# Kernel optimization log

Hardware: AMD Instinct MI355X
Metric: run time of the kernel (lower is better)

The kernel has to match this reference:

```python
import jax, jax.numpy as jnp
import numpy as np

B, L, K, D = 32, 1024, 1024, 1024

def setup_inputs() -> dict:
    key = jax.random.key(0)
    k1, k2, k3, k4, k5 = jax.random.split(key, 5)
    query = jax.random.normal(k1, (B, L, D), dtype=jnp.float32)
    context = jax.random.normal(k2, (B, K, D), dtype=jnp.float32)
    mask = jax.random.randint(k3, (B * L, K), 0, 2, dtype=jnp.int32)
    W_in = jax.random.normal(k4, (D, D), dtype=jnp.float32) * (D ** -0.5)
    W_out = jax.random.normal(k5, (D, 2 * D), dtype=jnp.float32) * ((2 * D) ** -0.5)
    return {"query": query, "context": context, "mask": mask, "W_in": W_in, "W_out": W_out}

def reference(query, context, mask, W_in, W_out):
    b, l, d = query.shape
    k = context.shape[1]
    # linear_in (general attention): q @ W_in.T
    q = jnp.einsum('bld,ed->ble', query, W_in)
    # attention scores [b, l, k]
    scores = jnp.einsum('bld,bkd->blk', q, context)
    # multiplicative-mask softmax with renormalization (masked_softmax, non-memory-efficient path)
    m = mask.astype(scores.dtype).reshape(b, l, k)
    w = jax.nn.softmax(scores * m, axis=-1) * m
    w = w / (jnp.sum(w, axis=-1, keepdims=True) + 1e-13)
    # mix attended context, concat with transformed query, project, tanh
    mix = jnp.einsum('blk,bkd->bld', w, context)
    combined = jnp.concatenate([mix, q], axis=-1)          # [b, l, 2d]
    out = jnp.tanh(jnp.einsum('blc,dc->bld', combined, W_out))
    return out
```

## Files before the change

### kernel.cpp

```cpp
#include <hip/hip_runtime.h>
#include <math.h>

typedef __bf16 bf16_t;
typedef __bf16 bf16x4 __attribute__((ext_vector_type(4)));
typedef __bf16 bf16x8 __attribute__((ext_vector_type(8)));
typedef _Float16 f16x4 __attribute__((ext_vector_type(4)));
typedef _Float16 f16x8 __attribute__((ext_vector_type(8)));
typedef float f32x4 __attribute__((ext_vector_type(4)));
typedef int i32x4 __attribute__((ext_vector_type(4)));

#define MFMA_BF16 __builtin_amdgcn_mfma_f32_16x16x32_bf16
#define MFMA_F16  __builtin_amdgcn_mfma_f32_16x16x32_f16

#define P_PRE                                         \
    __builtin_amdgcn_sched_barrier(0);                \
    __builtin_amdgcn_s_barrier();                     \
    asm volatile("s_waitcnt lgkmcnt(0)" ::: "memory");\
    __builtin_amdgcn_sched_barrier(0);                \
    __builtin_amdgcn_s_setprio(1)
#define P_POST                                        \
    __builtin_amdgcn_s_setprio(0);                    \
    __builtin_amdgcn_sched_barrier(0);                \
    __builtin_amdgcn_s_barrier()


__device__ __forceinline__ bf16_t to_bf16_rne(float x, float& rep) {
    unsigned u = __builtin_bit_cast(unsigned, x);
    unsigned r = u + 0x7fffu + ((u >> 16) & 1u);
    unsigned short h = (unsigned short)(r >> 16);
    rep = __builtin_bit_cast(float, ((unsigned)h) << 16);
    return __builtin_bit_cast(bf16_t, h);
}

__device__ __forceinline__ void g2l16(const void* g, void* l) {
    __builtin_amdgcn_global_load_lds(
        (const __attribute__((address_space(1))) unsigned int*)g,
        (__attribute__((address_space(3))) unsigned int*)l, 16, 0, 0);
}

__device__ __forceinline__ int lch(int r, int j) {
    return (r * 8 + (j ^ (r & 7))) * 8;
}

template <typename T>
__device__ __forceinline__ void stageA4(const T* __restrict__ gA, long long ldA,
                                        T* buf, int tid) {
    int wid = tid >> 6, lane = tid & 63;
#pragma unroll
    for (int i = 0; i < 4; ++i) {
        int cb = i * 512 + wid * 64;
        int c = cb + lane;
        int r = c >> 3, j = (c & 7) ^ (r & 7);
        g2l16(gA + (long long)r * ldA + j * 8, buf + (size_t)cb * 8);
    }
}

template <typename T>
__device__ __forceinline__ void stageB4(const T* __restrict__ gB, long long ldB,
                                        T* buf, int tid) {
    int wid = tid >> 6, lane = tid & 63;
#pragma unroll
    for (int i = 0; i < 4; ++i) {
        int cb = i * 512 + wid * 64;
        int c = cb + lane;
        int r = c >> 3, j = (c & 7) ^ (r & 7);
        g2l16(gB + (long long)r * ldB + j * 8, buf + 16384 + (size_t)cb * 8);
    }
}

template <typename T>
__device__ __forceinline__ void stage2(const T* __restrict__ gA, long long ldA,
                                       const T* __restrict__ gB, long long ldB,
                                       T* buf, int tid) {
    stageA4(gA, ldA, buf, tid);
    stageB4(gB, ldB, buf, tid);
}


__global__ __launch_bounds__(256) void split_int_k(const float* __restrict__ in,
                                                   bf16_t* __restrict__ out,
                                                   long long n4) {
    long long i = (long long)blockIdx.x * 256 + threadIdx.x;
    if (i >= n4) return;
    f32x4 v = ((const f32x4*)in)[i];
    bf16x4 hv, lv;
#pragma unroll
    for (int j = 0; j < 4; ++j) {
        float rep;
        hv[j] = to_bf16_rne(v[j], rep);
        float res = v[j] - rep;
        float rep2;
        lv[j] = to_bf16_rne(res, rep2);
    }
    long long row = i >> 8;
    int k = (int)(i & 255) * 4;
    long long base = row * 2048 + ((k >> 5) << 6) + (k & 31);
    *(bf16x4*)(out + base) = hv;
    *(bf16x4*)(out + base + 32) = lv;
}

__global__ __launch_bounds__(256) void cast_f16_k(const float* __restrict__ in,
                                                  _Float16* __restrict__ o, long long n4) {
    long long i = (long long)blockIdx.x * 256 + threadIdx.x;
    if (i >= n4) return;
    f32x4 v = ((const f32x4*)in)[i];
    f16x4 h;
#pragma unroll
    for (int j = 0; j < 4; ++j) h[j] = (_Float16)v[j];
    ((f16x4*)o)[i] = h;
}

__global__ __launch_bounds__(256) void prep_ctx_k(const float* __restrict__ ctx,
                                                  bf16_t* __restrict__ ctx_int,
                                                  _Float16* __restrict__ ctxT) {
    __shared__ _Float16 tl[32][33];
    int b = blockIdx.z;
    int k0 = blockIdx.x * 32, d0 = blockIdx.y * 32;
    const float* src = ctx + ((long long)b * 1024 + k0) * 1024 + d0;
    int x = threadIdx.x, y = threadIdx.y;
#pragma unroll
    for (int i = 0; i < 4; ++i) {
        int k = y + i * 8;
        float v = src[(long long)k * 1024 + x];
        float rep;
        bf16_t hb = to_bf16_rne(v, rep);
        float rep2;
        bf16_t lb = to_bf16_rne(v - rep, rep2);
        long long rb = ((long long)b * 1024 + k0 + k) * 2048 + d0 * 2 + x;
        ctx_int[rb] = hb;
        ctx_int[rb + 32] = lb;
        tl[x][k] = (_Float16)v;
    }
    __syncthreads();
    _Float16* dst = ctxT + ((long long)b * 1024 + d0) * 1024 + k0;
#pragma unroll
    for (int i = 0; i < 4; ++i) {
        int dd = y + i * 8;
        dst[(long long)dd * 1024 + x] = tl[dd][x];
    }
}

__global__ __launch_bounds__(256) void masked_softmax_k(const float* __restrict__ s,
                                                        const int* __restrict__ m,
                                                        _Float16* __restrict__ w) {
    long long row = blockIdx.x;
    const f32x4* sr = (const f32x4*)(s + row * 1024);
    const i32x4* mr = (const i32x4*)(m + row * 1024);
    f16x4* wr_ = (f16x4*)(w + row * 1024);
    int t = threadIdx.x;
    int lane = t & 63, wid = t >> 6;
    f32x4 v = sr[t];
    i32x4 mk = mr[t];
    float mx = -3.0e38f;
#pragma unroll
    for (int i = 0; i < 4; ++i)
        if (mk[i]) mx = fmaxf(mx, v[i]);
#pragma unroll
    for (int off = 32; off; off >>= 1) mx = fmaxf(mx, __shfl_xor(mx, off));
    __shared__ float rm[4], rs[4];
    if (!lane) rm[wid] = mx;
    __syncthreads();
    mx = fmaxf(fmaxf(rm[0], rm[1]), fmaxf(rm[2], rm[3]));
    float sum = 0.f;
    f32x4 e;
#pragma unroll
    for (int i = 0; i < 4; ++i) {
        e[i] = mk[i] ? expf(v[i] - mx) : 0.f;
        sum += e[i];
    }
#pragma unroll
    for (int off = 32; off; off >>= 1) sum += __shfl_xor(sum, off);
    if (!lane) rs[wid] = sum;
    __syncthreads();
    sum = rs[0] + rs[1] + rs[2] + rs[3];
    float inv = sum > 0.f ? 1.0f / sum : 0.f;
    f16x4 o;
#pragma unroll
    for (int i = 0; i < 4; ++i) o[i] = (_Float16)(e[i] * inv);
    wr_[t] = o;
}

template <int EPI>
__global__ __launch_bounds__(512, 2) void gemm_x3_256(
    const bf16_t* __restrict__ Aint, const bf16_t* __restrict__ Bint,
    long long sA, long long sB, long long sC, int nbx, int nby,
    float* __restrict__ Cs, bf16_t* __restrict__ Qint, _Float16* __restrict__ Qf) {
    __shared__ bf16_t lds[65536];
    const int NT = 32;
    int tid = threadIdx.x, lane = tid & 63, wid = tid >> 6;
    int wr = wid >> 2, wc = wid & 3;
    int nwg = gridDim.x;
    int bid = blockIdx.x;
    int lid = (bid & 7) * (nwg >> 3) + (bid >> 3);
    int by = lid % nby;
    int t2_ = lid / nby;
    int bx = t2_ % nbx;
    int z = t2_ / nbx;
    const bf16_t* At = Aint + (long long)z * sA + (long long)bx * 256 * 2048;
    const bf16_t* Bt = Bint + (long long)z * sB + (long long)by * 256 * 2048;
    stage2(At, 2048ll, Bt, 2048ll, lds, tid);
    stage2(At + 64, 2048ll, Bt + 64, 2048ll, lds + 32768, tid);
    f32x4 acc[8][4] = {};
    int l15 = lane & 15, l4 = lane >> 4;
    asm volatile("s_waitcnt vmcnt(8)" ::: "memory");
    __builtin_amdgcn_sched_barrier(0);
    __builtin_amdgcn_s_barrier();
    for (int t = 0; t < NT; ++t) {
        bf16_t* buf = lds + (size_t)(t & 1) * 32768;
        bf16_t* bufB = buf + 16384;
        const bf16_t* At2 = At + (long long)(t + 2) * 64;
        const bf16_t* Bt2 = Bt + (long long)(t + 2) * 64;
        bool st = (t + 2 < NT);
        bf16x8 bh[4], bl[4], ahA[2], alA[2];
#pragma unroll
        for (int n = 0; n < 4; ++n) {
            int rB = wc * 64 + n * 16 + l15;
            bh[n] = *(const bf16x8*)(bufB + lch(rB, l4));
            bl[n] = *(const bf16x8*)(bufB + lch(rB, 4 + l4));
        }
#pragma unroll
        for (int i = 0; i < 2; ++i) {
            int rA = wr * 128 + i * 16 + l15;
            ahA[i] = *(const bf16x8*)(buf + lch(rA, l4));
            alA[i] = *(const bf16x8*)(buf + lch(rA, 4 + l4));
        }
        P_PRE;
#pragma unroll
        for (int i = 0; i < 2; ++i)
#pragma unroll
            for (int n = 0; n < 4; ++n) {
                f32x4 a = acc[i][n];
                a = MFMA_BF16(ahA[i], bh[n], a, 0, 0, 0);
                a = MFMA_BF16(ahA[i], bl[n], a, 0, 0, 0);
                a = MFMA_BF16(alA[i], bh[n], a, 0, 0, 0);
                acc[i][n] = a;
            }
        P_POST;
        bf16x8 ahB[2], alB[2], ahC[2], alC[2];
#pragma unroll
        for (int i = 0; i < 2; ++i) {
            int rA = wr * 128 + (2 + i) * 16 + l15;
            ahB[i] = *(const bf16x8*)(buf + lch(rA, l4));
            alB[i] = *(const bf16x8*)(buf + lch(rA, 4 + l4));
        }
#pragma unroll
        for (int i = 0; i < 2; ++i) {
            int rA = wr * 128 + (4 + i) * 16 + l15;
            ahC[i] = *(const bf16x8*)(buf + lch(rA, l4));
            alC[i] = *(const bf16x8*)(buf + lch(rA, 4 + l4));
        }
        P_PRE;
#pragma unroll
        for (int i = 0; i < 2; ++i)
#pragma unroll
            for (int n = 0; n < 4; ++n) {
                f32x4 a = acc[2 + i][n];
                a = MFMA_BF16(ahB[i], bh[n], a, 0, 0, 0);
                a = MFMA_BF16(ahB[i], bl[n], a, 0, 0, 0);
                a = MFMA_BF16(alB[i], bh[n], a, 0, 0, 0);
                acc[2 + i][n] = a;
            }
        P_POST;
        bf16x8 ahD[2], alD[2];
#pragma unroll
        for (int i = 0; i < 2; ++i) {
            int rA = wr * 128 + (6 + i) * 16 + l15;
            ahD[i] = *(const bf16x8*)(buf + lch(rA, l4));
            alD[i] = *(const bf16x8*)(buf + lch(rA, 4 + l4));
        }
        if (st) stageB4(Bt2, 2048ll, buf, tid);
        P_PRE;
#pragma unroll
        for (int i = 0; i < 2; ++i)
#pragma unroll
            for (int n = 0; n < 4; ++n) {
                f32x4 a = acc[4 + i][n];
                a = MFMA_BF16(ahC[i], bh[n], a, 0, 0, 0);
                a = MFMA_BF16(ahC[i], bl[n], a, 0, 0, 0);
                a = MFMA_BF16(alC[i], bh[n], a, 0, 0, 0);
                acc[4 + i][n] = a;
            }
        P_POST;
        if (st) stageA4(At2, 2048ll, buf, tid);
        __builtin_amdgcn_s_setprio(1);
#pragma unroll
        for (int i = 0; i < 2; ++i)
#pragma unroll
            for (int n = 0; n < 4; ++n) {
                f32x4 a = acc[6 + i][n];
                a = MFMA_BF16(ahD[i], bh[n], a, 0, 0, 0);
                a = MFMA_BF16(ahD[i], bl[n], a, 0, 0, 0);
                a = MFMA_BF16(alD[i], bh[n], a, 0, 0, 0);
                acc[6 + i][n] = a;
            }
        __builtin_amdgcn_s_setprio(0);
        __builtin_amdgcn_sched_barrier(0);
        if (t + 2 < NT) {
            asm volatile("s_waitcnt vmcnt(8)" ::: "memory");
        } else if (t + 1 < NT) {
            asm volatile("s_waitcnt vmcnt(0)" ::: "memory");
        }
        __builtin_amdgcn_sched_barrier(0);
        __builtin_amdgcn_s_barrier();
    }
    int r0 = bx * 256 + wr * 128 + (l4 << 2);
    int c0 = by * 256 + wc * 64 + l15;
#pragma unroll
    for (int m = 0; m < 8; ++m)
#pragma unroll
        for (int n = 0; n < 4; ++n)
#pragma unroll
            for (int j = 0; j < 4; ++j) {
                int r = r0 + m * 16 + j;
                int c = c0 + n * 16;
                float v = acc[m][n][j];
                if (EPI == 0) {
                    Cs[(long long)z * sC + (long long)r * 1024 + c] = v;
                } else {
                    float rep;
                    bf16_t hb = to_bf16_rne(v, rep);
                    float res = v - rep;
                    float rep2;
                    bf16_t lb = to_bf16_rne(res, rep2);
                    long long rb = (long long)r * 2048 + ((c >> 5) << 6) + (c & 31);
                    Qint[rb] = hb;
                    Qint[rb + 32] = lb;
                    Qf[(long long)r * 1024 + c] = (_Float16)v;
                }
            }
}

template <int EPI>
__global__ __launch_bounds__(512, 2) void gemm_f16_256(
    const _Float16* __restrict__ A1, const _Float16* __restrict__ A2,
    const _Float16* __restrict__ B,
    long long ldA, long long ldB, long long sA, long long sB, long long sC,
    int NT, int swt, int nbx, int nby,
    _Float16* __restrict__ Cm, float* __restrict__ Co) {
    __shared__ _Float16 lds[65536];
    int tid = threadIdx.x, lane = tid & 63, wid = tid >> 6;
    int wr = wid >> 2, wc = wid & 3;
    int nwg = gridDim.x;
    int bid = blockIdx.x;
    int lid = (bid & 7) * (nwg >> 3) + (bid >> 3);
    int by = lid % nby;
    int t2_ = lid / nby;
    int bx = t2_ % nbx;
    int z = t2_ / nbx;
    const _Float16* A1t = A1 + (long long)z * sA + (long long)bx * 256 * ldA;
    const _Float16* A2t = A2 + (long long)bx * 256 * ldA;
    const _Float16* Bt = B + (long long)z * sB + (long long)by * 256 * ldB;
    stage2((0 < swt) ? A1t : A2t, ldA, Bt, ldB, lds, tid);
    stage2((1 < swt) ? A1t + 64 : A2t + (long long)(1 - swt) * 64, ldA, Bt + 64, ldB,
           lds + 32768, tid);
    f32x4 acc[8][4] = {};
    int l15 = lane & 15, l4 = lane >> 4;
    asm volatile("s_waitcnt vmcnt(8)" ::: "memory");
    __builtin_amdgcn_sched_barrier(0);
    __builtin_amdgcn_s_barrier();
    for (int t = 0; t < NT; ++t) {
        _Float16* buf = lds + (size_t)(t & 1) * 32768;
        _Float16* bufB = buf + 16384;
        int tt = t + 2;
        bool st = (tt < NT);
        const _Float16* gA2 =
            (tt < swt) ? A1t + (long long)tt * 64 : A2t + (long long)(tt - swt) * 64;
        const _Float16* gB2 = Bt + (long long)tt * 64;
        f16x8 bfr[4][2], aA[2][2];
#pragma unroll
        for (int n = 0; n < 4; ++n) {
            int rB = wc * 64 + n * 16 + l15;
#pragma unroll
            for (int ks = 0; ks < 2; ++ks)
                bfr[n][ks] = *(const f16x8*)(bufB + lch(rB, ks * 4 + l4));
        }
#pragma unroll
        for (int i = 0; i < 2; ++i) {
            int rA = wr * 128 + i * 16 + l15;
#pragma unroll
            for (int ks = 0; ks < 2; ++ks)
                aA[i][ks] = *(const f16x8*)(buf + lch(rA, ks * 4 + l4));
        }
        P_PRE;
#pragma unroll
        for (int i = 0; i < 2; ++i)
#pragma unroll
            for (int n = 0; n < 4; ++n) {
                f32x4 v = acc[i][n];
                v = MFMA_F16(aA[i][0], bfr[n][0], v, 0, 0, 0);
                v = MFMA_F16(aA[i][1], bfr[n][1], v, 0, 0, 0);
                acc[i][n] = v;
            }
        P_POST;
        f16x8 aB[2][2], aC[2][2];
#pragma unroll
        for (int i = 0; i < 2; ++i) {
            int rA = wr * 128 + (2 + i) * 16 + l15;
#pragma unroll
            for (int ks = 0; ks < 2; ++ks)
                aB[i][ks] = *(const f16x8*)(buf + lch(rA, ks * 4 + l4));
        }
#pragma unroll
        for (int i = 0; i < 2; ++i) {
            int rA = wr * 128 + (4 + i) * 16 + l15;
#pragma unroll
            for (int ks = 0; ks < 2; ++ks)
                aC[i][ks] = *(const f16x8*)(buf + lch(rA, ks * 4 + l4));
        }
        P_PRE;
#pragma unroll
        for (int i = 0; i < 2; ++i)
#pragma unroll
            for (int n = 0; n < 4; ++n) {
                f32x4 v = acc[2 + i][n];
                v = MFMA_F16(aB[i][0], bfr[n][0], v, 0, 0, 0);
                v = MFMA_F16(aB[i][1], bfr[n][1], v, 0, 0, 0);
                acc[2 + i][n] = v;
            }
        P_POST;
        f16x8 aD[2][2];
#pragma unroll
        for (int i = 0; i < 2; ++i) {
            int rA = wr * 128 + (6 + i) * 16 + l15;
#pragma unroll
            for (int ks = 0; ks < 2; ++ks)
                aD[i][ks] = *(const f16x8*)(buf + lch(rA, ks * 4 + l4));
        }
        if (st) stageB4(gB2, ldB, buf, tid);
        P_PRE;
#pragma unroll
        for (int i = 0; i < 2; ++i)
#pragma unroll
            for (int n = 0; n < 4; ++n) {
                f32x4 v = acc[4 + i][n];
                v = MFMA_F16(aC[i][0], bfr[n][0], v, 0, 0, 0);
                v = MFMA_F16(aC[i][1], bfr[n][1], v, 0, 0, 0);
                acc[4 + i][n] = v;
            }
        P_POST;
        if (st) stageA4(gA2, ldA, buf, tid);
        __builtin_amdgcn_s_setprio(1);
#pragma unroll
        for (int i = 0; i < 2; ++i)
#pragma unroll
            for (int n = 0; n < 4; ++n) {
                f32x4 v = acc[6 + i][n];
                v = MFMA_F16(aD[i][0], bfr[n][0], v, 0, 0, 0);
                v = MFMA_F16(aD[i][1], bfr[n][1], v, 0, 0, 0);
                acc[6 + i][n] = v;
            }
        __builtin_amdgcn_s_setprio(0);
        __builtin_amdgcn_sched_barrier(0);
        if (t + 2 < NT) {
            asm volatile("s_waitcnt vmcnt(8)" ::: "memory");
        } else if (t + 1 < NT) {
            asm volatile("s_waitcnt vmcnt(0)" ::: "memory");
        }
        __builtin_amdgcn_sched_barrier(0);
        __builtin_amdgcn_s_barrier();
    }
    int r0 = bx * 256 + wr * 128 + (l4 << 2);
    int c0 = by * 256 + wc * 64 + l15;
#pragma unroll
    for (int m = 0; m < 8; ++m)
#pragma unroll
        for (int n = 0; n < 4; ++n)
#pragma unroll
            for (int j = 0; j < 4; ++j) {
                int r = r0 + m * 16 + j;
                int c = c0 + n * 16;
                float v = acc[m][n][j];
                if (EPI == 0) {
                    Cm[(long long)z * sC + (long long)r * 1024 + c] = (_Float16)v;
                } else {
                    Co[(long long)r * 1024 + c] = tanhf(v);
                }
            }
}


extern "C" void kernel_launch(void* const* d_in, const int* in_sizes, int n_in,
                              void* d_out, int out_size, void* d_ws, size_t ws_size,
                              hipStream_t stream) {
    const float* query = (const float*)d_in[0];
    const float* ctx = (const float*)d_in[1];
    const int* mask = (const int*)d_in[2];
    const float* Win = (const float*)d_in[3];
    const float* Wout = (const float*)d_in[4];
    float* outp = (float*)d_out;

    const long long MB = 1048576ll;
    int G = 1;
    if ((long long)ws_size >= 512 * MB) G = 32;
    else if ((long long)ws_size >= 256 * MB) G = 16;
    else if ((long long)ws_size >= 128 * MB) G = 8;
    else if ((long long)ws_size >= 64 * MB) G = 4;
    else if ((long long)ws_size >= 32 * MB) G = 2;

    char* p = (char*)d_ws;
    const long long R = (long long)G * 1024;
    bf16_t* qint = (bf16_t*)p; p += 4 * G * MB;
    _Float16* qf = (_Float16*)p; p += 2 * G * MB;
    char* slabA = p; p += 4 * G * MB;
    bf16_t* win_int = (bf16_t*)slabA;
    bf16_t* ctx_int = (bf16_t*)slabA;
    _Float16* wf = (_Float16*)slabA;
    _Float16* mixf = (_Float16*)(slabA + 2 * G * MB);
    _Float16* ctxT = (_Float16*)p; p += 2 * G * MB;
    char* slabC = p;
    bf16_t* qs_int = (bf16_t*)slabC;
    float* scores = (float*)slabC;
    _Float16* woutf = (_Float16*)slabC;

    const long long LD = 1048576ll;

    for (int b0 = 0; b0 < 32; b0 += G) {
        const float* qsrc = query + (long long)b0 * LD;
        const float* csrc = ctx + (long long)b0 * LD;
        split_int_k<<<1024, 256, 0, stream>>>(Win, win_int, 262144ll);
        split_int_k<<<(int)R, 256, 0, stream>>>(qsrc, qs_int, R * 256);
        gemm_x3_256<1><<<16 * G, 512, 0, stream>>>(
            qs_int, win_int, 0, 0, 0, 4 * G, 4, nullptr, qint, qf);
        prep_ctx_k<<<dim3(32, 32, G), dim3(32, 8, 1), 0, stream>>>(csrc, ctx_int, ctxT);
        gemm_x3_256<0><<<16 * G, 512, 0, stream>>>(
            qint, ctx_int, 2097152ll, 2097152ll, 1048576ll, 4, 4,
            scores, nullptr, nullptr);
        masked_softmax_k<<<(int)R, 256, 0, stream>>>(
            scores, mask + (long long)b0 * 1024 * 1024, wf);
        cast_f16_k<<<2048, 256, 0, stream>>>(Wout, woutf, 524288ll);
        gemm_f16_256<0><<<16 * G, 512, 0, stream>>>(
            wf, wf, ctxT, 1024ll, 1024ll, 1048576ll, 1048576ll, 1048576ll,
            16, 1 << 20, 4, 4, mixf, nullptr);
        gemm_f16_256<1><<<16 * G, 512, 0, stream>>>(
            mixf, qf, woutf, 1024ll, 2048ll, 0, 0, 0,
            32, 16, 4 * G, 4, nullptr, outp + (long long)b0 * LD);
    }
}
```

Before: 762.3 us.

## Replace per-phase barriers with lgkmcnt-pipelined LDS fragment loads in GEMM loops

Both GEMM main loops drop the workgroup barrier and full lgkmcnt(0) wait around each MFMA phase. A fragments for later phases are now issued ahead of time, and partial lgkmcnt waits let LDS reads overlap MFMAs of earlier phases. One barrier before the global-to-LDS staging of both A and B tiles replaces the two separate staging points. This cuts barrier stalls, but it moves all staging of the next tile into the final phase and raises register pressure from the extra in-flight fragments.

After: 783.8 us. 1.03x slower.

```diff
diff --git a/kernel.cpp b/kernel.cpp
--- a/kernel.cpp
+++ b/kernel.cpp
@@ -12,16 +12,12 @@
 #define MFMA_BF16 __builtin_amdgcn_mfma_f32_16x16x32_bf16
 #define MFMA_F16  __builtin_amdgcn_mfma_f32_16x16x32_f16
 
-#define P_PRE                                         \
-    __builtin_amdgcn_sched_barrier(0);                \
-    __builtin_amdgcn_s_barrier();                     \
-    asm volatile("s_waitcnt lgkmcnt(0)" ::: "memory");\
-    __builtin_amdgcn_sched_barrier(0);                \
-    __builtin_amdgcn_s_setprio(1)
-#define P_POST                                        \
-    __builtin_amdgcn_s_setprio(0);                    \
-    __builtin_amdgcn_sched_barrier(0);                \
-    __builtin_amdgcn_s_barrier()
+#define SB0 __builtin_amdgcn_sched_barrier(0)
+#define LGKM(n)                                                  \
+    do {                                                         \
+        asm volatile("s_waitcnt lgkmcnt(" #n ")" ::: "memory");  \
+        __builtin_amdgcn_sched_barrier(0);                       \
+    } while (0)
 
 
 __device__ __forceinline__ bf16_t to_bf16_rne(float x, float& rep) {
@@ -43,8 +39,9 @@
 }
 
 template <typename T>
-__device__ __forceinline__ void stageA4(const T* __restrict__ gA, long long ldA,
-                                        T* buf, int tid) {
+__device__ __forceinline__ void stage2(const T* __restrict__ gA, long long ldA,
+                                       const T* __restrict__ gB, long long ldB,
+                                       T* buf, int tid) {
     int wid = tid >> 6, lane = tid & 63;
 #pragma unroll
     for (int i = 0; i < 4; ++i) {
@@ -53,12 +50,6 @@
         int r = c >> 3, j = (c & 7) ^ (r & 7);
         g2l16(gA + (long long)r * ldA + j * 8, buf + (size_t)cb * 8);
     }
-}
-
-template <typename T>
-__device__ __forceinline__ void stageB4(const T* __restrict__ gB, long long ldB,
-                                        T* buf, int tid) {
-    int wid = tid >> 6, lane = tid & 63;
 #pragma unroll
     for (int i = 0; i < 4; ++i) {
         int cb = i * 512 + wid * 64;
@@ -66,14 +57,6 @@
         int r = c >> 3, j = (c & 7) ^ (r & 7);
         g2l16(gB + (long long)r * ldB + j * 8, buf + 16384 + (size_t)cb * 8);
     }
-}
-
-template <typename T>
-__device__ __forceinline__ void stage2(const T* __restrict__ gA, long long ldA,
-                                       const T* __restrict__ gB, long long ldB,
-                                       T* buf, int tid) {
-    stageA4(gA, ldA, buf, tid);
-    stageB4(gB, ldB, buf, tid);
 }
 
 
@@ -203,104 +186,115 @@
     f32x4 acc[8][4] = {};
     int l15 = lane & 15, l4 = lane >> 4;
     asm volatile("s_waitcnt vmcnt(8)" ::: "memory");
-    __builtin_amdgcn_sched_barrier(0);
+    SB0;
     __builtin_amdgcn_s_barrier();
     for (int t = 0; t < NT; ++t) {
         bf16_t* buf = lds + (size_t)(t & 1) * 32768;
         bf16_t* bufB = buf + 16384;
-        const bf16_t* At2 = At + (long long)(t + 2) * 64;
-        const bf16_t* Bt2 = Bt + (long long)(t + 2) * 64;
         bool st = (t + 2 < NT);
-        bf16x8 bh[4], bl[4], ahA[2], alA[2];
+        bf16x8 bh[4], bl[4];
 #pragma unroll
         for (int n = 0; n < 4; ++n) {
             int rB = wc * 64 + n * 16 + l15;
             bh[n] = *(const bf16x8*)(bufB + lch(rB, l4));
             bl[n] = *(const bf16x8*)(bufB + lch(rB, 4 + l4));
         }
+        bf16x8 ah0[2], al0[2];
 #pragma unroll
         for (int i = 0; i < 2; ++i) {
             int rA = wr * 128 + i * 16 + l15;
-            ahA[i] = *(const bf16x8*)(buf + lch(rA, l4));
-            alA[i] = *(const bf16x8*)(buf + lch(rA, 4 + l4));
-        }
-        P_PRE;
-#pragma unroll
-        for (int i = 0; i < 2; ++i)
-#pragma unroll
-            for (int n = 0; n < 4; ++n) {
-                f32x4 a = acc[i][n];
-                a = MFMA_BF16(ahA[i], bh[n], a, 0, 0, 0);
-                a = MFMA_BF16(ahA[i], bl[n], a, 0, 0, 0);
-                a = MFMA_BF16(alA[i], bh[n], a, 0, 0, 0);
-                acc[i][n] = a;
-            }
-        P_POST;
-        bf16x8 ahB[2], alB[2], ahC[2], alC[2];
+            ah0[i] = *(const bf16x8*)(buf + lch(rA, l4));
+            al0[i] = *(const bf16x8*)(buf + lch(rA, 4 + l4));
+        }
+        SB0;
+        bf16x8 ah1[2], al1[2];
 #pragma unroll
         for (int i = 0; i < 2; ++i) {
             int rA = wr * 128 + (2 + i) * 16 + l15;
-            ahB[i] = *(const bf16x8*)(buf + lch(rA, l4));
-            alB[i] = *(const bf16x8*)(buf + lch(rA, 4 + l4));
-        }
+            ah1[i] = *(const bf16x8*)(buf + lch(rA, l4));
+            al1[i] = *(const bf16x8*)(buf + lch(rA, 4 + l4));
+        }
+        SB0;
+        LGKM(4);
+        bf16x8 ah2[2], al2[2];
 #pragma unroll
         for (int i = 0; i < 2; ++i) {
             int rA = wr * 128 + (4 + i) * 16 + l15;
-            ahC[i] = *(const bf16x8*)(buf + lch(rA, l4));
-            alC[i] = *(const bf16x8*)(buf + lch(rA, 4 + l4));
-        }
-        P_PRE;
-#pragma unroll
-        for (int i = 0; i < 2; ++i)
-#pragma unroll
-            for (int n = 0; n < 4; ++n) {
-                f32x4 a = acc[2 + i][n];
-                a = MFMA_BF16(ahB[i], bh[n], a, 0, 0, 0);
-                a = MFMA_BF16(ahB[i], bl[n], a, 0, 0, 0);
-                a = MFMA_BF16(alB[i], bh[n], a, 0, 0, 0);
-                acc[2 + i][n] = a;
-            }
-        P_POST;
-        bf16x8 ahD[2], alD[2];
+            ah2[i] = *(const bf16x8*)(buf + lch(rA, l4));
+            al2[i] = *(const bf16x8*)(buf + lch(rA, 4 + l4));
+        }
+        SB0;
+        __builtin_amdgcn_s_setprio(1);
+#pragma unroll
+        for (int i = 0; i < 2; ++i)
+#pragma unroll
+            for (int n = 0; n < 4; ++n) {
+                f32x4 a = acc[i][n];
+                a = MFMA_BF16(ah0[i], bh[n], a, 0, 0, 0);
+                a = MFMA_BF16(ah0[i], bl[n], a, 0, 0, 0);
+                a = MFMA_BF16(al0[i], bh[n], a, 0, 0, 0);
+                acc[i][n] = a;
+            }
+        __builtin_amdgcn_s_setprio(0);
+        LGKM(4);
+        bf16x8 ah3[2], al3[2];
 #pragma unroll
         for (int i = 0; i < 2; ++i) {
             int rA = wr * 128 + (6 + i) * 16 + l15;
-            ahD[i] = *(const bf16x8*)(buf + lch(rA, l4));
-            alD[i] = *(const bf16x8*)(buf + lch(rA, 4 + l4));
-        }
-        if (st) stageB4(Bt2, 2048ll, buf, tid);
-        P_PRE;
+            ah3[i] = *(const bf16x8*)(buf + lch(rA, l4));
+            al3[i] = *(const bf16x8*)(buf + lch(rA, 4 + l4));
+        }
+        SB0;
+        __builtin_amdgcn_s_setprio(1);
+#pragma unroll
+        for (int i = 0; i < 2; ++i)
+#pragma unroll
+            for (int n = 0; n < 4; ++n) {
+                f32x4 a = acc[2 + i][n];
+                a = MFMA_BF16(ah1[i], bh[n], a, 0, 0, 0);
+                a = MFMA_BF16(ah1[i], bl[n], a, 0, 0, 0);
+                a = MFMA_BF16(al1[i], bh[n], a, 0, 0, 0);
+                acc[2 + i][n] = a;
+            }
+        __builtin_amdgcn_s_setprio(0);
+        LGKM(4);
+        __builtin_amdgcn_s_setprio(1);
 #pragma unroll
         for (int i = 0; i < 2; ++i)
 #pragma unroll
             for (int n = 0; n < 4; ++n) {
                 f32x4 a = acc[4 + i][n];
-                a = MFMA_BF16(ahC[i], bh[n], a, 0, 0, 0);
-                a = MFMA_BF16(ahC[i], bl[n], a, 0, 0, 0);
-                a = MFMA_BF16(alC[i], bh[n], a, 0, 0, 0);
+                a = MFMA_BF16(ah2[i], bh[n], a, 0, 0, 0);
+                a = MFMA_BF16(ah2[i], bl[n], a, 0, 0, 0);
+                a = MFMA_BF16(al2[i], bh[n], a, 0, 0, 0);
                 acc[4 + i][n] = a;
             }
-        P_POST;
-        if (st) stageA4(At2, 2048ll, buf, tid);
+        __builtin_amdgcn_s_setprio(0);
+        LGKM(0);
+        __builtin_amdgcn_s_barrier();
+        SB0;
+        if (st)
+            stage2(At + (long long)(t + 2) * 64, 2048ll,
+                   Bt + (long long)(t + 2) * 64, 2048ll, buf, tid);
         __builtin_amdgcn_s_setprio(1);
 #pragma unroll
         for (int i = 0; i < 2; ++i)
 #pragma unroll
             for (int n = 0; n < 4; ++n) {
                 f32x4 a = acc[6 + i][n];
-                a = MFMA_BF16(ahD[i], bh[n], a, 0, 0, 0);
-                a = MFMA_BF16(ahD[i], bl[n], a, 0, 0, 0);
-                a = MFMA_BF16(alD[i], bh[n], a, 0, 0, 0);
+                a = MFMA_BF16(ah3[i], bh[n], a, 0, 0, 0);
+                a = MFMA_BF16(ah3[i], bl[n], a, 0, 0, 0);
+                a = MFMA_BF16(al3[i], bh[n], a, 0, 0, 0);
                 acc[6 + i][n] = a;
             }
         __builtin_amdgcn_s_setprio(0);
-        __builtin_amdgcn_sched_barrier(0);
+        SB0;
         if (t + 2 < NT) {
             asm volatile("s_waitcnt vmcnt(8)" ::: "memory");
         } else if (t + 1 < NT) {
             asm volatile("s_waitcnt vmcnt(0)" ::: "memory");
         }
-        __builtin_amdgcn_sched_barrier(0);
+        SB0;
         __builtin_amdgcn_s_barrier();
     }
     int r0 = bx * 256 + wr * 128 + (l4 << 2);
@@ -356,7 +350,7 @@
     f32x4 acc[8][4] = {};
     int l15 = lane & 15, l4 = lane >> 4;
     asm volatile("s_waitcnt vmcnt(8)" ::: "memory");
-    __builtin_amdgcn_sched_barrier(0);
+    SB0;
     __builtin_amdgcn_s_barrier();
     for (int t = 0; t < NT; ++t) {
         _Float16* buf = lds + (size_t)(t & 1) * 32768;
@@ -366,7 +360,7 @@
         const _Float16* gA2 =
             (tt < swt) ? A1t + (long long)tt * 64 : A2t + (long long)(tt - swt) * 64;
         const _Float16* gB2 = Bt + (long long)tt * 64;
-        f16x8 bfr[4][2], aA[2][2];
+        f16x8 bfr[4][2];
 #pragma unroll
         for (int n = 0; n < 4; ++n) {
             int rB = wc * 64 + n * 16 + l15;
@@ -374,89 +368,100 @@
             for (int ks = 0; ks < 2; ++ks)
                 bfr[n][ks] = *(const f16x8*)(bufB + lch(rB, ks * 4 + l4));
         }
-#pragma unroll
-        for (int i = 0; i < 2; ++i) {
-            int rA = wr * 128 + i * 16 + l15;
-#pragma unroll
-            for (int ks = 0; ks < 2; ++ks)
-                aA[i][ks] = *(const f16x8*)(buf + lch(rA, ks * 4 + l4));
-        }
-        P_PRE;
+        f16x8 a0[2][2];
+#pragma unroll
+        for (int i = 0; i < 2; ++i)
+#pragma unroll
+            for (int ks = 0; ks < 2; ++ks) {
+                int rA = wr * 128 + i * 16 + l15;
+                a0[i][ks] = *(const f16x8*)(buf + lch(rA, ks * 4 + l4));
+            }
+        SB0;
+        f16x8 a1[2][2];
+#pragma unroll
+        for (int i = 0; i < 2; ++i)
+#pragma unroll
+            for (int ks = 0; ks < 2; ++ks) {
+                int rA = wr * 128 + (2 + i) * 16 + l15;
+                a1[i][ks] = *(const f16x8*)(buf + lch(rA, ks * 4 + l4));
+            }
+        SB0;
+        LGKM(4);
+        f16x8 a2[2][2];
+#pragma unroll
+        for (int i = 0; i < 2; ++i)
+#pragma unroll
+            for (int ks = 0; ks < 2; ++ks) {
+                int rA = wr * 128 + (4 + i) * 16 + l15;
+                a2[i][ks] = *(const f16x8*)(buf + lch(rA, ks * 4 + l4));
+            }
+        SB0;
+        __builtin_amdgcn_s_setprio(1);
 #pragma unroll
         for (int i = 0; i < 2; ++i)
 #pragma unroll
             for (int n = 0; n < 4; ++n) {
                 f32x4 v = acc[i][n];
-                v = MFMA_F16(aA[i][0], bfr[n][0], v, 0, 0, 0);
-                v = MFMA_F16(aA[i][1], bfr[n][1], v, 0, 0, 0);
+                v = MFMA_F16(a0[i][0], bfr[n][0], v, 0, 0, 0);
+                v = MFMA_F16(a0[i][1], bfr[n][1], v, 0, 0, 0);
                 acc[i][n] = v;
             }
-        P_POST;
-        f16x8 aB[2][2], aC[2][2];
-#pragma unroll
-        for (int i = 0; i < 2; ++i) {
-            int rA = wr * 128 + (2 + i) * 16 + l15;
-#pragma unroll
-            for (int ks = 0; ks < 2; ++ks)
-                aB[i][ks] = *(const f16x8*)(buf + lch(rA, ks * 4 + l4));
-        }
-#pragma unroll
-        for (int i = 0; i < 2; ++i) {
-            int rA = wr * 128 + (4 + i) * 16 + l15;
-#pragma unroll
-            for (int ks = 0; ks < 2; ++ks)
-                aC[i][ks] = *(const f16x8*)(buf + lch(rA, ks * 4 + l4));
-        }
-        P_PRE;
+        __builtin_amdgcn_s_setprio(0);
+        LGKM(4);
+        f16x8 a3[2][2];
+#pragma unroll
+        for (int i = 0; i < 2; ++i)
+#pragma unroll
+            for (int ks = 0; ks < 2; ++ks) {
+                int rA = wr * 128 + (6 + i) * 16 + l15;
+                a3[i][ks] = *(const f16x8*)(buf + lch(rA, ks * 4 + l4));
+            }
+        SB0;
+        __builtin_amdgcn_s_setprio(1);
 #pragma unroll
         for (int i = 0; i < 2; ++i)
 #pragma unroll
             for (int n = 0; n < 4; ++n) {
                 f32x4 v = acc[2 + i][n];
-                v = MFMA_F16(aB[i][0], bfr[n][0], v, 0, 0, 0);
-                v = MFMA_F16(aB[i][1], bfr[n][1], v, 0, 0, 0);
+                v = MFMA_F16(a1[i][0], bfr[n][0], v, 0, 0, 0);
+                v = MFMA_F16(a1[i][1], bfr[n][1], v, 0, 0, 0);
                 acc[2 + i][n] = v;
             }
-        P_POST;
-        f16x8 aD[2][2];
-#pragma unroll
-        for (int i = 0; i < 2; ++i) {
-            int rA = wr * 128 + (6 + i) * 16 + l15;
-#pragma unroll
-            for (int ks = 0; ks < 2; ++ks)
-                aD[i][ks] = *(const f16x8*)(buf + lch(rA, ks * 4 + l4));
-        }
-        if (st) stageB4(gB2, ldB, buf, tid);
-        P_PRE;
+        __builtin_amdgcn_s_setprio(0);
+        LGKM(4);
+        __builtin_amdgcn_s_setprio(1);
 #pragma unroll
         for (int i = 0; i < 2; ++i)
 #pragma unroll
             for (int n = 0; n < 4; ++n) {
                 f32x4 v = acc[4 + i][n];
-                v = MFMA_F16(aC[i][0], bfr[n][0], v, 0, 0, 0);
-                v = MFMA_F16(aC[i][1], bfr[n][1], v, 0, 0, 0);
+                v = MFMA_F16(a2[i][0], bfr[n][0], v, 0, 0, 0);
+                v = MFMA_F16(a2[i][1], bfr[n][1], v, 0, 0, 0);
                 acc[4 + i][n] = v;
             }
-        P_POST;
-        if (st) stageA4(gA2, ldA, buf, tid);
+        __builtin_amdgcn_s_setprio(0);
+        LGKM(0);
+        __builtin_amdgcn_s_barrier();
+        SB0;
+        if (st) stage2(gA2, ldA, gB2, ldB, buf, tid);
         __builtin_amdgcn_s_setprio(1);
 #pragma unroll
         for (int i = 0; i < 2; ++i)
 #pragma unroll
             for (int n = 0; n < 4; ++n) {
                 f32x4 v = acc[6 + i][n];
-                v = MFMA_F16(aD[i][0], bfr[n][0], v, 0, 0, 0);
-                v = MFMA_F16(aD[i][1], bfr[n][1], v, 0, 0, 0);
+                v = MFMA_F16(a3[i][0], bfr[n][0], v, 0, 0, 0);
+                v = MFMA_F16(a3[i][1], bfr[n][1], v, 0, 0, 0);
                 acc[6 + i][n] = v;
             }
         __builtin_amdgcn_s_setprio(0);
-        __builtin_amdgcn_sched_barrier(0);
+        SB0;
         if (t + 2 < NT) {
             asm volatile("s_waitcnt vmcnt(8)" ::: "memory");
         } else if (t + 1 < NT) {
             asm volatile("s_waitcnt vmcnt(0)" ::: "memory");
         }
-        __builtin_amdgcn_sched_barrier(0);
+        SB0;
         __builtin_amdgcn_s_barrier();
     }
     int r0 = bx * 256 + wr * 128 + (l4 << 2);
```

## Fuse fp32-to-bf16 split into x3 GEMM loads and mask into scores epilogue

Applied to the files above, without the earlier changes.

The x3 bf16 GEMM now loads fp32 query/context tiles directly into registers and splits them into hi/lo bf16 while writing LDS. This removes the separate split_int_k pass over query and the ctx_int output of the context prep kernel. The mask is applied in the scores GEMM epilogue by writing a large negative sentinel, so the softmax kernel no longer reads the mask. The cost is more VALU work and register-staged loads inside the GEMM main loop, a changed vmcnt pipeline, and reordered workspace buffers.

New measurement: 781.3 us. +2.5%, slower.

```diff
diff --git a/kernel.cpp b/kernel.cpp
--- a/kernel.cpp
+++ b/kernel.cpp
@@ -11,6 +11,7 @@
 
 #define MFMA_BF16 __builtin_amdgcn_mfma_f32_16x16x32_bf16
 #define MFMA_F16  __builtin_amdgcn_mfma_f32_16x16x32_f16
+#define SB0 __builtin_amdgcn_sched_barrier(0)
 
 #define P_PRE                                         \
     __builtin_amdgcn_sched_barrier(0);                \
@@ -42,9 +43,47 @@
     return (r * 8 + (j ^ (r & 7))) * 8;
 }
 
-template <typename T>
-__device__ __forceinline__ void stageA4(const T* __restrict__ gA, long long ldA,
-                                        T* buf, int tid) {
+__device__ __forceinline__ void stageG(const bf16_t* __restrict__ g, bf16_t* dst,
+                                       int tid) {
+    int wid = tid >> 6, lane = tid & 63;
+#pragma unroll
+    for (int i = 0; i < 4; ++i) {
+        int cb = i * 512 + wid * 64;
+        int c = cb + lane;
+        int r = c >> 3, j = (c & 7) ^ (r & 7);
+        g2l16(g + (long long)r * 2048 + j * 8, dst + (size_t)cb * 8);
+    }
+}
+
+__device__ __forceinline__ void ldf32(const float* __restrict__ g, int tid,
+                                      f32x4* v) {
+    int r = tid >> 1, h = tid & 1;
+    const f32x4* s = (const f32x4*)(g + (long long)r * 1024 + h * 16);
+#pragma unroll
+    for (int i = 0; i < 4; ++i) v[i] = s[i];
+}
+
+__device__ __forceinline__ void wrsplit(bf16_t* dst, int tid, const f32x4* v) {
+    int r = tid >> 1, h = tid & 1;
+    bf16x8 H[2], L[2];
+#pragma unroll
+    for (int e = 0; e < 16; ++e) {
+        float x = v[e >> 2][e & 3];
+        float rep;
+        bf16_t hb = to_bf16_rne(x, rep);
+        float r2;
+        bf16_t lb = to_bf16_rne(x - rep, r2);
+        H[e >> 3][e & 7] = hb;
+        L[e >> 3][e & 7] = lb;
+    }
+    *(bf16x8*)(dst + lch(r, h * 2)) = H[0];
+    *(bf16x8*)(dst + lch(r, h * 2 + 1)) = H[1];
+    *(bf16x8*)(dst + lch(r, 4 + h * 2)) = L[0];
+    *(bf16x8*)(dst + lch(r, 4 + h * 2 + 1)) = L[1];
+}
+
+__device__ __forceinline__ void stageA4h(const _Float16* __restrict__ gA, long long ldA,
+                                         _Float16* buf, int tid) {
     int wid = tid >> 6, lane = tid & 63;
 #pragma unroll
     for (int i = 0; i < 4; ++i) {
@@ -54,10 +93,8 @@
         g2l16(gA + (long long)r * ldA + j * 8, buf + (size_t)cb * 8);
     }
 }
-
-template <typename T>
-__device__ __forceinline__ void stageB4(const T* __restrict__ gB, long long ldB,
-                                        T* buf, int tid) {
+__device__ __forceinline__ void stageB4h(const _Float16* __restrict__ gB, long long ldB,
+                                         _Float16* buf, int tid) {
     int wid = tid >> 6, lane = tid & 63;
 #pragma unroll
     for (int i = 0; i < 4; ++i) {
@@ -67,13 +104,11 @@
         g2l16(gB + (long long)r * ldB + j * 8, buf + 16384 + (size_t)cb * 8);
     }
 }
-
-template <typename T>
-__device__ __forceinline__ void stage2(const T* __restrict__ gA, long long ldA,
-                                       const T* __restrict__ gB, long long ldB,
-                                       T* buf, int tid) {
-    stageA4(gA, ldA, buf, tid);
-    stageB4(gB, ldB, buf, tid);
+__device__ __forceinline__ void stage2h(const _Float16* __restrict__ gA, long long ldA,
+                                        const _Float16* __restrict__ gB, long long ldB,
+                                        _Float16* buf, int tid) {
+    stageA4h(gA, ldA, buf, tid);
+    stageB4h(gB, ldB, buf, tid);
 }
 
 
@@ -110,9 +145,8 @@
     ((f16x4*)o)[i] = h;
 }
 
-__global__ __launch_bounds__(256) void prep_ctx_k(const float* __restrict__ ctx,
-                                                  bf16_t* __restrict__ ctx_int,
-                                                  _Float16* __restrict__ ctxT) {
+__global__ __launch_bounds__(256) void transpose_ctx_k(const float* __restrict__ ctx,
+                                                       _Float16* __restrict__ ctxT) {
     __shared__ _Float16 tl[32][33];
     int b = blockIdx.z;
     int k0 = blockIdx.x * 32, d0 = blockIdx.y * 32;
@@ -121,15 +155,7 @@
 #pragma unroll
     for (int i = 0; i < 4; ++i) {
         int k = y + i * 8;
-        float v = src[(long long)k * 1024 + x];
-        float rep;
-        bf16_t hb = to_bf16_rne(v, rep);
-        float rep2;
-        bf16_t lb = to_bf16_rne(v - rep, rep2);
-        long long rb = ((long long)b * 1024 + k0 + k) * 2048 + d0 * 2 + x;
-        ctx_int[rb] = hb;
-        ctx_int[rb + 32] = lb;
-        tl[x][k] = (_Float16)v;
+        tl[x][k] = (_Float16)src[(long long)k * 1024 + x];
     }
     __syncthreads();
     _Float16* dst = ctxT + ((long long)b * 1024 + d0) * 1024 + k0;
@@ -141,20 +167,14 @@
 }
 
 __global__ __launch_bounds__(256) void masked_softmax_k(const float* __restrict__ s,
-                                                        const int* __restrict__ m,
                                                         _Float16* __restrict__ w) {
     long long row = blockIdx.x;
     const f32x4* sr = (const f32x4*)(s + row * 1024);
-    const i32x4* mr = (const i32x4*)(m + row * 1024);
     f16x4* wr_ = (f16x4*)(w + row * 1024);
     int t = threadIdx.x;
     int lane = t & 63, wid = t >> 6;
     f32x4 v = sr[t];
-    i32x4 mk = mr[t];
-    float mx = -3.0e38f;
-#pragma unroll
-    for (int i = 0; i < 4; ++i)
-        if (mk[i]) mx = fmaxf(mx, v[i]);
+    float mx = fmaxf(fmaxf(v[0], v[1]), fmaxf(v[2], v[3]));
 #pragma unroll
     for (int off = 32; off; off >>= 1) mx = fmaxf(mx, __shfl_xor(mx, off));
     __shared__ float rm[4], rs[4];
@@ -165,7 +185,7 @@
     f32x4 e;
 #pragma unroll
     for (int i = 0; i < 4; ++i) {
-        e[i] = mk[i] ? expf(v[i] - mx) : 0.f;
+        e[i] = expf(v[i] - mx);
         sum += e[i];
     }
 #pragma unroll
@@ -173,17 +193,18 @@
     if (!lane) rs[wid] = sum;
     __syncthreads();
     sum = rs[0] + rs[1] + rs[2] + rs[3];
-    float inv = sum > 0.f ? 1.0f / sum : 0.f;
+    float inv = (mx < -1.0e38f) ? 0.f : 1.0f / sum;
     f16x4 o;
 #pragma unroll
     for (int i = 0; i < 4; ++i) o[i] = (_Float16)(e[i] * inv);
     wr_[t] = o;
 }
 
-template <int EPI>
+template <int EPI, bool F32A>
 __global__ __launch_bounds__(512, 2) void gemm_x3_256(
-    const bf16_t* __restrict__ Aint, const bf16_t* __restrict__ Bint,
-    long long sA, long long sB, long long sC, int nbx, int nby,
+    const bf16_t* __restrict__ Gint, const float* __restrict__ Fsrc,
+    const int* __restrict__ Mk,
+    long long sG, long long sF, long long sC, int nbx, int nby,
     float* __restrict__ Cs, bf16_t* __restrict__ Qint, _Float16* __restrict__ Qf) {
     __shared__ bf16_t lds[65536];
     const int NT = 32;
@@ -196,21 +217,31 @@
     int t2_ = lid / nby;
     int bx = t2_ % nbx;
     int z = t2_ / nbx;
-    const bf16_t* At = Aint + (long long)z * sA + (long long)bx * 256 * 2048;
-    const bf16_t* Bt = Bint + (long long)z * sB + (long long)by * 256 * 2048;
-    stage2(At, 2048ll, Bt, 2048ll, lds, tid);
-    stage2(At + 64, 2048ll, Bt + 64, 2048ll, lds + 32768, tid);
+    const bf16_t* Gt = Gint + (long long)z * sG + (long long)(F32A ? by : bx) * 256 * 2048;
+    const float* Ft = Fsrc + (long long)z * sF + (long long)(F32A ? bx : by) * 256 * 1024;
+    const int FOFF = F32A ? 0 : 16384;
+    const int GOFF = F32A ? 16384 : 0;
+    {
+        f32x4 v[4];
+        ldf32(Ft, tid, v);
+        wrsplit(lds + FOFF, tid, v);
+        ldf32(Ft + 32, tid, v);
+        wrsplit(lds + 32768 + FOFF, tid, v);
+        stageG(Gt, lds + GOFF, tid);
+        stageG(Gt + 64, lds + 32768 + GOFF, tid);
+        asm volatile("s_waitcnt lgkmcnt(0) vmcnt(0)" ::: "memory");
+        SB0;
+        __builtin_amdgcn_s_barrier();
+    }
     f32x4 acc[8][4] = {};
     int l15 = lane & 15, l4 = lane >> 4;
-    asm volatile("s_waitcnt vmcnt(8)" ::: "memory");
-    __builtin_amdgcn_sched_barrier(0);
-    __builtin_amdgcn_s_barrier();
     for (int t = 0; t < NT; ++t) {
         bf16_t* buf = lds + (size_t)(t & 1) * 32768;
         bf16_t* bufB = buf + 16384;
-        const bf16_t* At2 = At + (long long)(t + 2) * 64;
-        const bf16_t* Bt2 = Bt + (long long)(t + 2) * 64;
         bool st = (t + 2 < NT);
+        f32x4 v[4];
+        if (st) ldf32(Ft + (t + 2) * 32, tid, v);
+        SB0;
         bf16x8 bh[4], bl[4], ahA[2], alA[2];
 #pragma unroll
         for (int n = 0; n < 4; ++n) {
@@ -268,7 +299,7 @@
             ahD[i] = *(const bf16x8*)(buf + lch(rA, l4));
             alD[i] = *(const bf16x8*)(buf + lch(rA, 4 + l4));
         }
-        if (st) stageB4(Bt2, 2048ll, buf, tid);
+        if (st && F32A) stageG(Gt + (long long)(t + 2) * 64, buf + GOFF, tid);
         P_PRE;
 #pragma unroll
         for (int i = 0; i < 2; ++i)
@@ -281,7 +312,8 @@
                 acc[4 + i][n] = a;
             }
         P_POST;
-        if (st) stageA4(At2, 2048ll, buf, tid);
+        if (st && !F32A) stageG(Gt + (long long)(t + 2) * 64, buf + GOFF, tid);
+        if (st) wrsplit(buf + FOFF, tid, v);
         __builtin_amdgcn_s_setprio(1);
 #pragma unroll
         for (int i = 0; i < 2; ++i)
@@ -294,17 +326,20 @@
                 acc[6 + i][n] = a;
             }
         __builtin_amdgcn_s_setprio(0);
-        __builtin_amdgcn_sched_barrier(0);
-        if (t + 2 < NT) {
-            asm volatile("s_waitcnt vmcnt(8)" ::: "memory");
-        } else if (t + 1 < NT) {
+        SB0;
+        asm volatile("s_waitcnt lgkmcnt(0)" ::: "memory");
+        SB0;
+        if (st) {
+            asm volatile("s_waitcnt vmcnt(4)" ::: "memory");
+        } else {
             asm volatile("s_waitcnt vmcnt(0)" ::: "memory");
         }
-        __builtin_amdgcn_sched_barrier(0);
+        SB0;
         __builtin_amdgcn_s_barrier();
     }
     int r0 = bx * 256 + wr * 128 + (l4 << 2);
     int c0 = by * 256 + wc * 64 + l15;
+    const int* mrow = (EPI == 0) ? (Mk + (long long)z * 1048576ll) : nullptr;
 #pragma unroll
     for (int m = 0; m < 8; ++m)
 #pragma unroll
@@ -315,7 +350,8 @@
                 int c = c0 + n * 16;
                 float v = acc[m][n][j];
                 if (EPI == 0) {
-                    Cs[(long long)z * sC + (long long)r * 1024 + c] = v;
+                    int mv = mrow[(long long)r * 1024 + c];
+                    Cs[(long long)z * sC + (long long)r * 1024 + c] = mv ? v : -3.0e38f;
                 } else {
                     float rep;
                     bf16_t hb = to_bf16_rne(v, rep);
@@ -350,13 +386,13 @@
     const _Float16* A1t = A1 + (long long)z * sA + (long long)bx * 256 * ldA;
     const _Float16* A2t = A2 + (long long)bx * 256 * ldA;
     const _Float16* Bt = B + (long long)z * sB + (long long)by * 256 * ldB;
-    stage2((0 < swt) ? A1t : A2t, ldA, Bt, ldB, lds, tid);
-    stage2((1 < swt) ? A1t + 64 : A2t + (long long)(1 - swt) * 64, ldA, Bt + 64, ldB,
-           lds + 32768, tid);
+    stage2h((0 < swt) ? A1t : A2t, ldA, Bt, ldB, lds, tid);
+    stage2h((1 < swt) ? A1t + 64 : A2t + (long long)(1 - swt) * 64, ldA, Bt + 64, ldB,
+            lds + 32768, tid);
     f32x4 acc[8][4] = {};
     int l15 = lane & 15, l4 = lane >> 4;
     asm volatile("s_waitcnt vmcnt(8)" ::: "memory");
-    __builtin_amdgcn_sched_barrier(0);
+    SB0;
     __builtin_amdgcn_s_barrier();
     for (int t = 0; t < NT; ++t) {
         _Float16* buf = lds + (size_t)(t & 1) * 32768;
@@ -386,10 +422,10 @@
         for (int i = 0; i < 2; ++i)
 #pragma unroll
             for (int n = 0; n < 4; ++n) {
-                f32x4 v = acc[i][n];
-                v = MFMA_F16(aA[i][0], bfr[n][0], v, 0, 0, 0);
-                v = MFMA_F16(aA[i][1], bfr[n][1], v, 0, 0, 0);
-                acc[i][n] = v;
+                f32x4 vv = acc[i][n];
+                vv = MFMA_F16(aA[i][0], bfr[n][0], vv, 0, 0, 0);
+                vv = MFMA_F16(aA[i][1], bfr[n][1], vv, 0, 0, 0);
+                acc[i][n] = vv;
             }
         P_POST;
         f16x8 aB[2][2], aC[2][2];
@@ -412,10 +448,10 @@
         for (int i = 0; i < 2; ++i)
 #pragma unroll
             for (int n = 0; n < 4; ++n) {
-                f32x4 v = acc[2 + i][n];
-                v = MFMA_F16(aB[i][0], bfr[n][0], v, 0, 0, 0);
-                v = MFMA_F16(aB[i][1], bfr[n][1], v, 0, 0, 0);
-                acc[2 + i][n] = v;
+                f32x4 vv = acc[2 + i][n];
+                vv = MFMA_F16(aB[i][0], bfr[n][0], vv, 0, 0, 0);
+                vv = MFMA_F16(aB[i][1], bfr[n][1], vv, 0, 0, 0);
+                acc[2 + i][n] = vv;
             }
         P_POST;
         f16x8 aD[2][2];
@@ -426,37 +462,37 @@
             for (int ks = 0; ks < 2; ++ks)
                 aD[i][ks] = *(const f16x8*)(buf + lch(rA, ks * 4 + l4));
         }
-        if (st) stageB4(gB2, ldB, buf, tid);
+        if (st) stageB4h(gB2, ldB, buf, tid);
         P_PRE;
 #pragma unroll
         for (int i = 0; i < 2; ++i)
 #pragma unroll
             for (int n = 0; n < 4; ++n) {
-                f32x4 v = acc[4 + i][n];
-                v = MFMA_F16(aC[i][0], bfr[n][0], v, 0, 0, 0);
-                v = MFMA_F16(aC[i][1], bfr[n][1], v, 0, 0, 0);
-                acc[4 + i][n] = v;
+                f32x4 vv = acc[4 + i][n];
+                vv = MFMA_F16(aC[i][0], bfr[n][0], vv, 0, 0, 0);
+                vv = MFMA_F16(aC[i][1], bfr[n][1], vv, 0, 0, 0);
+                acc[4 + i][n] = vv;
             }
         P_POST;
-        if (st) stageA4(gA2, ldA, buf, tid);
+        if (st) stageA4h(gA2, ldA, buf, tid);
         __builtin_amdgcn_s_setprio(1);
 #pragma unroll
         for (int i = 0; i < 2; ++i)
 #pragma unroll
             for (int n = 0; n < 4; ++n) {
-                f32x4 v = acc[6 + i][n];
-                v = MFMA_F16(aD[i][0], bfr[n][0], v, 0, 0, 0);
-                v = MFMA_F16(aD[i][1], bfr[n][1], v, 0, 0, 0);
-                acc[6 + i][n] = v;
+                f32x4 vv = acc[6 + i][n];
+                vv = MFMA_F16(aD[i][0], bfr[n][0], vv, 0, 0, 0);
+                vv = MFMA_F16(aD[i][1], bfr[n][1], vv, 0, 0, 0);
+                acc[6 + i][n] = vv;
             }
         __builtin_amdgcn_s_setprio(0);
-        __builtin_amdgcn_sched_barrier(0);
+        SB0;
         if (t + 2 < NT) {
             asm volatile("s_waitcnt vmcnt(8)" ::: "memory");
         } else if (t + 1 < NT) {
             asm volatile("s_waitcnt vmcnt(0)" ::: "memory");
         }
-        __builtin_amdgcn_sched_barrier(0);
+        SB0;
         __builtin_amdgcn_s_barrier();
     }
     int r0 = bx * 256 + wr * 128 + (l4 << 2);
@@ -501,16 +537,12 @@
     const long long R = (long long)G * 1024;
     bf16_t* qint = (bf16_t*)p; p += 4 * G * MB;
     _Float16* qf = (_Float16*)p; p += 2 * G * MB;
-    char* slabA = p; p += 4 * G * MB;
-    bf16_t* win_int = (bf16_t*)slabA;
-    bf16_t* ctx_int = (bf16_t*)slabA;
-    _Float16* wf = (_Float16*)slabA;
-    _Float16* mixf = (_Float16*)(slabA + 2 * G * MB);
     _Float16* ctxT = (_Float16*)p; p += 2 * G * MB;
-    char* slabC = p;
-    bf16_t* qs_int = (bf16_t*)slabC;
-    float* scores = (float*)slabC;
-    _Float16* woutf = (_Float16*)slabC;
+    _Float16* wf = (_Float16*)p; p += 2 * G * MB;
+    _Float16* mixf = (_Float16*)p; p += 2 * G * MB;
+    float* scores = (float*)p;
+    bf16_t* win_int = (bf16_t*)scores;
+    _Float16* woutf = (_Float16*)qint;
 
     const long long LD = 1048576ll;
 
@@ -518,15 +550,13 @@
         const float* qsrc = query + (long long)b0 * LD;
         const float* csrc = ctx + (long long)b0 * LD;
         split_int_k<<<1024, 256, 0, stream>>>(Win, win_int, 262144ll);
-        split_int_k<<<(int)R, 256, 0, stream>>>(qsrc, qs_int, R * 256);
-        gemm_x3_256<1><<<16 * G, 512, 0, stream>>>(
-            qs_int, win_int, 0, 0, 0, 4 * G, 4, nullptr, qint, qf);
-        prep_ctx_k<<<dim3(32, 32, G), dim3(32, 8, 1), 0, stream>>>(csrc, ctx_int, ctxT);
-        gemm_x3_256<0><<<16 * G, 512, 0, stream>>>(
-            qint, ctx_int, 2097152ll, 2097152ll, 1048576ll, 4, 4,
-            scores, nullptr, nullptr);
-        masked_softmax_k<<<(int)R, 256, 0, stream>>>(
-            scores, mask + (long long)b0 * 1024 * 1024, wf);
+        gemm_x3_256<1, true><<<16 * G, 512, 0, stream>>>(
+            win_int, qsrc, nullptr, 0, 0, 0, 4 * G, 4, nullptr, qint, qf);
+        transpose_ctx_k<<<dim3(32, 32, G), dim3(32, 8, 1), 0, stream>>>(csrc, ctxT);
+        gemm_x3_256<0, false><<<16 * G, 512, 0, stream>>>(
+            qint, csrc, mask + (long long)b0 * LD,
+            2097152ll, 1048576ll, 1048576ll, 4, 4, scores, nullptr, nullptr);
+        masked_softmax_k<<<(int)R, 256, 0, stream>>>(scores, wf);
         cast_f16_k<<<2048, 256, 0, stream>>>(Wout, woutf, 524288ll);
         gemm_f16_256<0><<<16 * G, 512, 0, stream>>>(
             wf, wf, ctxT, 1024ll, 1024ll, 1048576ll, 1048576ll, 1048576ll,
```
